# Kernel tuning notes

Measured on AMD Instinct MI355X. Metric: run time of the kernel, lower is better.

Reference implementation:

```python
import jax, jax.numpy as jnp
import numpy as np

B, S, HD = 2, 2048, 2048   # batch, seq_len, hidden_dim
NH = 16                    # num_heads
DH = HD // NH              # head_dim = 128
L = 512                    # kv_latent_dim
WINDOW = 128               # sliding window size
SINKS = 16                 # persistent (attention-sink) tokens
KTOP = 64                  # dynamic top-k tokens selected outside window/sinks
FORGET_P = 0.1             # stochastic forgetting probability


def setup_inputs() -> dict:
    key = jax.random.key(0)
    ks = jax.random.split(key, 7)
    s = 0.02
    x = jax.random.normal(ks[0], (B, S, HD), jnp.float32)
    Wq = jax.random.normal(ks[1], (HD, HD), jnp.float32) * s
    Wc = jax.random.normal(ks[2], (HD, L), jnp.float32) * s   # kv_latent_proj
    Wk = jax.random.normal(ks[3], (L, HD), jnp.float32) * s   # k_proj (latent -> hidden)
    Wv = jax.random.normal(ks[4], (L, HD), jnp.float32) * s   # v_proj (latent -> hidden)
    Wo = jax.random.normal(ks[5], (HD, HD), jnp.float32) * s  # out_proj
    forget_mask = jax.random.bernoulli(ks[6], FORGET_P, (B, NH, S, S))
    return dict(x=x, Wq=Wq, Wc=Wc, Wk=Wk, Wv=Wv, Wo=Wo, forget_mask=forget_mask)


def reference(x, Wq, Wc, Wk, Wv, Wo, forget_mask):
    scale = DH ** -0.5
    # projections: queries from x, keys/values through low-rank latent
    q = (x @ Wq).reshape(B, S, NH, DH).transpose(0, 2, 1, 3)   # [B,H,S,D]
    c = x @ Wc                                                  # [B,S,L] latent KV
    k = (c @ Wk).reshape(B, S, NH, DH).transpose(0, 2, 1, 3)
    v = (c @ Wv).reshape(B, S, NH, DH).transpose(0, 2, 1, 3)

    scores = jnp.einsum('bhqd,bhkd->bhqk', q, k) * scale        # [B,H,S,S]

    i = jnp.arange(S)[:, None]
    j = jnp.arange(S)[None, :]
    causal = j <= i
    # static pattern: sink tokens + sliding window (always attended)
    base = causal & ((j < SINKS) | ((i - j) < WINDOW))          # [S,S]

    NEG = jnp.finfo(scores.dtype).min
    # candidates for dynamic top-k: causal positions NOT already in window/sinks
    cand = jnp.where(causal & ~base, scores, NEG)
    vals, idx = jax.lax.top_k(cand, KTOP)                       # [B,H,S,K]

    # scatter top-k indices into a boolean mask (invalid = NEG-filled entries)
    N = B * NH * S
    rows = jnp.arange(N)[:, None]
    tk = jnp.zeros((N, S), dtype=bool).at[rows, idx.reshape(N, KTOP)].set(
        (vals > NEG / 2).reshape(N, KTOP))
    tk = tk.reshape(B, NH, S, S)

    # stochastic forgetting applies only to the dynamically selected tokens;
    # sinks and the sliding window are never forgotten
    allowed = base[None, None] | (tk & ~forget_mask)

    attn = jax.nn.softmax(jnp.where(allowed, scores, NEG), axis=-1)
    o = jnp.einsum('bhqk,bhkd->bhqd', attn, v)                  # [B,H,S,D]
    o = o.transpose(0, 2, 1, 3).reshape(B, S, HD)
    return o @ Wo
```

## Files before the change

kernel.cpp:

```cpp
#include <hip/hip_runtime.h>
#include <hip/hip_fp16.h>

#define B_ 2
#define S_ 2048
#define HD_ 2048
#define NH_ 16
#define DH_ 128
#define L_ 512
#define WINDOW_ 128
#define SINKS_ 16
#define KTOP_ 64
#define KST 2052

typedef __attribute__((ext_vector_type(4))) float f32x4;
typedef __attribute__((ext_vector_type(8))) __bf16 bf16x8;

__device__ inline unsigned short f2bf(float f) {
  unsigned int u = __float_as_uint(f);
  unsigned int r = (u + 0x7FFFu + ((u >> 16) & 1u)) >> 16;
  return (unsigned short)r;
}
__device__ inline float bf2f(unsigned short u) {
  unsigned int x = ((unsigned int)u) << 16;
  return __uint_as_float(x);
}
__device__ inline unsigned int mono(float f) {
  unsigned int u = __float_as_uint(f);
  return (u & 0x80000000u) ? ~u : (u | 0x80000000u);
}
__device__ inline float dq16(unsigned int k16) {
  unsigned int m = (k16 << 16) | 0x8000u;
  unsigned int u = (m & 0x80000000u) ? (m & 0x7fffffffu) : ~m;
  return __uint_as_float(u);
}
__device__ inline void gl16(const unsigned short* g, unsigned short* l) {
  __builtin_amdgcn_global_load_lds(
      (const __attribute__((address_space(1))) unsigned int*)g,
      (__attribute__((address_space(3))) unsigned int*)l, 16, 0, 0);
}

__global__ __launch_bounds__(256) void cast_f32(const float* __restrict__ in,
                                                unsigned short* __restrict__ hi,
                                                int n) {
  int i = (blockIdx.x * 256 + threadIdx.x) * 4;
  int stride = gridDim.x * 256 * 4;
  for (; i < n; i += stride) {
    float4 v = *(const float4*)(in + i);
    ushort4 h;
    h.x = f2bf(v.x); h.y = f2bf(v.y); h.z = f2bf(v.z); h.w = f2bf(v.w);
    *(ushort4*)(hi + i) = h;
  }
}

__global__ __launch_bounds__(256) void transpose_cast(const float* __restrict__ W,
                                                      unsigned short* __restrict__ WT,
                                                      int K, int N) {
  __shared__ unsigned short th[32][33];
  int n0 = blockIdx.x * 32, k0 = blockIdx.y * 32;
  int t = threadIdx.x;
  int cx = t & 31, ry = t >> 5;
#pragma unroll
  for (int it = 0; it < 4; ++it) {
    int kk = ry + it * 8;
    th[cx][kk] = f2bf(W[(size_t)(k0 + kk) * N + n0 + cx]);
  }
  __syncthreads();
#pragma unroll
  for (int it = 0; it < 4; ++it) {
    int nn = ry + it * 8;
    WT[(size_t)(n0 + nn) * K + k0 + cx] = th[nn][cx];
  }
}

__global__ __launch_bounds__(256) void transpose_split(const float* __restrict__ W,
                                                       unsigned short* __restrict__ WTh,
                                                       unsigned short* __restrict__ WTl,
                                                       int K, int N) {
  __shared__ unsigned short th[32][33];
  __shared__ unsigned short tl[32][33];
  int n0 = blockIdx.x * 32, k0 = blockIdx.y * 32;
  int t = threadIdx.x;
  int cx = t & 31, ry = t >> 5;
#pragma unroll
  for (int it = 0; it < 4; ++it) {
    int kk = ry + it * 8;
    float v = W[(size_t)(k0 + kk) * N + n0 + cx];
    unsigned short h = f2bf(v);
    th[cx][kk] = h;
    tl[cx][kk] = f2bf(v - bf2f(h));
  }
  __syncthreads();
#pragma unroll
  for (int it = 0; it < 4; ++it) {
    int nn = ry + it * 8;
    WTh[(size_t)(n0 + nn) * K + k0 + cx] = th[nn][cx];
    WTl[(size_t)(n0 + nn) * K + k0 + cx] = tl[nn][cx];
  }
}

__global__ __launch_bounds__(256) void gemm_c64(const unsigned short* __restrict__ Ah,
                                                const unsigned short* __restrict__ Bth,
                                                const unsigned short* __restrict__ Btl,
                                                unsigned short* __restrict__ Chi,
                                                int M, int N, int K) {
  __shared__ unsigned short lAh[64 * 32];
  __shared__ unsigned short lBh[128 * 32];
  __shared__ unsigned short lBl[128 * 32];
  int t = threadIdx.x;
  int row0 = blockIdx.x * 64, col0 = blockIdx.y * 128;
  int w = t >> 6, lane = t & 63;
  int wm = w >> 1, wn = w & 1;
  int lr = lane & 15, g = lane >> 4;

  f32x4 acc[2][4] = {};

  for (int kt = 0; kt < K; kt += 32) {
    {
      int Lb = w * 1024;
      int L = Lb + lane * 16;
      int rr = L >> 6, kc = (L & 63) >> 1;
      size_t offA = (size_t)(row0 + rr) * K + kt + kc;
      gl16(Ah + offA, lAh + Lb / 2);
      int Lb0 = (2 * w) * 1024;
      int L0 = Lb0 + lane * 16;
      int rr0 = L0 >> 6, kc0 = (L0 & 63) >> 1;
      size_t offB0 = (size_t)(col0 + rr0) * K + kt + kc0;
      gl16(Bth + offB0, lBh + Lb0 / 2);
      gl16(Btl + offB0, lBl + Lb0 / 2);
      int Lb1 = (2 * w + 1) * 1024;
      int L1 = Lb1 + lane * 16;
      int rr1 = L1 >> 6, kc1 = (L1 & 63) >> 1;
      size_t offB1 = (size_t)(col0 + rr1) * K + kt + kc1;
      gl16(Bth + offB1, lBh + Lb1 / 2);
      gl16(Btl + offB1, lBl + Lb1 / 2);
    }
    __syncthreads();
    bf16x8 af[2], bgh[4], bgl[4];
#pragma unroll
    for (int m = 0; m < 2; ++m)
      af[m] = *(const bf16x8*)&lAh[(wm * 32 + m * 16 + lr) * 32 + g * 8];
#pragma unroll
    for (int n = 0; n < 4; ++n) {
      bgh[n] = *(const bf16x8*)&lBh[(wn * 64 + n * 16 + lr) * 32 + g * 8];
      bgl[n] = *(const bf16x8*)&lBl[(wn * 64 + n * 16 + lr) * 32 + g * 8];
    }
#pragma unroll
    for (int m = 0; m < 2; ++m)
#pragma unroll
      for (int n = 0; n < 4; ++n) {
        acc[m][n] = __builtin_amdgcn_mfma_f32_16x16x32_bf16(af[m], bgh[n], acc[m][n], 0, 0, 0);
        acc[m][n] = __builtin_amdgcn_mfma_f32_16x16x32_bf16(af[m], bgl[n], acc[m][n], 0, 0, 0);
      }
    __syncthreads();
  }

#pragma unroll
  for (int m = 0; m < 2; ++m)
#pragma unroll
    for (int n = 0; n < 4; ++n)
#pragma unroll
      for (int r2 = 0; r2 < 4; ++r2) {
        int row = row0 + wm * 32 + m * 16 + g * 4 + r2;
        int col = col0 + wn * 64 + n * 16 + lr;
        Chi[(size_t)row * N + col] = f2bf(acc[m][n][r2]);
      }
}

__global__ __launch_bounds__(256) void gemm_1term(const unsigned short* __restrict__ Ah,
                                                  const unsigned short* __restrict__ Bth,
                                                  unsigned short* __restrict__ Chi,
                                                  int M, int N, int K, float oscale) {
  __shared__ unsigned short lA[128 * 32];
  __shared__ unsigned short lB[128 * 32];
  int t = threadIdx.x;
  int row0 = blockIdx.x * 128, col0 = blockIdx.y * 128;
  int w = t >> 6, lane = t & 63;
  int wm = w >> 1, wn = w & 1;
  int lr = lane & 15, g = lane >> 4;

  f32x4 acc[4][4] = {};

  for (int kt = 0; kt < K; kt += 32) {
#pragma unroll
    for (int cc = 0; cc < 2; ++cc) {
      int chunk = cc * 4 + w;
      int Lb = chunk * 1024;
      int L = Lb + lane * 16;
      int rr = L >> 6;
      int kc = (L & 63) >> 1;
      size_t offA = (size_t)(row0 + rr) * K + kt + kc;
      size_t offB = (size_t)(col0 + rr) * K + kt + kc;
      gl16(Ah + offA, lA + Lb / 2);
      gl16(Bth + offB, lB + Lb / 2);
    }
    __syncthreads();
    bf16x8 af[4], bg[4];
#pragma unroll
    for (int m = 0; m < 4; ++m) af[m] = *(const bf16x8*)&lA[(wm * 64 + m * 16 + lr) * 32 + g * 8];
#pragma unroll
    for (int n = 0; n < 4; ++n) bg[n] = *(const bf16x8*)&lB[(wn * 64 + n * 16 + lr) * 32 + g * 8];
#pragma unroll
    for (int m = 0; m < 4; ++m)
#pragma unroll
      for (int n = 0; n < 4; ++n)
        acc[m][n] = __builtin_amdgcn_mfma_f32_16x16x32_bf16(af[m], bg[n], acc[m][n], 0, 0, 0);
    __syncthreads();
  }

#pragma unroll
  for (int m = 0; m < 4; ++m)
#pragma unroll
    for (int n = 0; n < 4; ++n)
#pragma unroll
      for (int r2 = 0; r2 < 4; ++r2) {
        int row = row0 + wm * 64 + m * 16 + g * 4 + r2;
        int col = col0 + wn * 64 + n * 16 + lr;
        Chi[(size_t)row * N + col] = f2bf(acc[m][n][r2] * oscale);
      }
}

__global__ __launch_bounds__(256) void gemm_1h(const unsigned short* __restrict__ Ah,
                                               const unsigned short* __restrict__ Bth,
                                               unsigned short* __restrict__ Ch,
                                               int M, int N, int K) {
  __shared__ unsigned short lA[128 * 32];
  __shared__ unsigned short lB[128 * 32];
  int t = threadIdx.x;
  int row0 = blockIdx.x * 128, col0 = blockIdx.y * 128;
  int w = t >> 6, lane = t & 63;
  int wm = w >> 1, wn = w & 1;
  int lr = lane & 15, g = lane >> 4;

  f32x4 acc[4][4] = {};

  for (int kt = 0; kt < K; kt += 32) {
#pragma unroll
    for (int cc = 0; cc < 2; ++cc) {
      int chunk = cc * 4 + w;
      int Lb = chunk * 1024;
      int L = Lb + lane * 16;
      int rr = L >> 6;
      int kc = (L & 63) >> 1;
      size_t offA = (size_t)(row0 + rr) * K + kt + kc;
      size_t offB = (size_t)(col0 + rr) * K + kt + kc;
      gl16(Ah + offA, lA + Lb / 2);
      gl16(Bth + offB, lB + Lb / 2);
    }
    __syncthreads();
    bf16x8 af[4], bg[4];
#pragma unroll
    for (int m = 0; m < 4; ++m) af[m] = *(const bf16x8*)&lA[(wm * 64 + m * 16 + lr) * 32 + g * 8];
#pragma unroll
    for (int n = 0; n < 4; ++n) bg[n] = *(const bf16x8*)&lB[(wn * 64 + n * 16 + lr) * 32 + g * 8];
#pragma unroll
    for (int m = 0; m < 4; ++m)
#pragma unroll
      for (int n = 0; n < 4; ++n)
        acc[m][n] = __builtin_amdgcn_mfma_f32_16x16x32_bf16(af[m], bg[n], acc[m][n], 0, 0, 0);
    __syncthreads();
  }

#pragma unroll
  for (int m = 0; m < 4; ++m)
#pragma unroll
    for (int n = 0; n < 4; ++n)
#pragma unroll
      for (int r2 = 0; r2 < 4; ++r2) {
        int row = row0 + wm * 64 + m * 16 + g * 4 + r2;
        int col = col0 + wn * 64 + n * 16 + lr;
        __half hv = __float2half(acc[m][n][r2]);
        Ch[(size_t)row * N + col] = __half_as_ushort(hv);
      }
}

__global__ __launch_bounds__(256) void gemm_1f(const unsigned short* __restrict__ Ah,
                                               const unsigned short* __restrict__ Bth,
                                               float* __restrict__ Cf,
                                               int M, int N, int K) {
  __shared__ unsigned short lA[128 * 32];
  __shared__ unsigned short lB[128 * 32];
  int t = threadIdx.x;
  int row0 = blockIdx.x * 128, col0 = blockIdx.y * 128;
  int w = t >> 6, lane = t & 63;
  int wm = w >> 1, wn = w & 1;
  int lr = lane & 15, g = lane >> 4;

  f32x4 acc[4][4] = {};

  for (int kt = 0; kt < K; kt += 32) {
#pragma unroll
    for (int cc = 0; cc < 2; ++cc) {
      int chunk = cc * 4 + w;
      int Lb = chunk * 1024;
      int L = Lb + lane * 16;
      int rr = L >> 6;
      int kc = (L & 63) >> 1;
      size_t offA = (size_t)(row0 + rr) * K + kt + kc;
      size_t offB = (size_t)(col0 + rr) * K + kt + kc;
      gl16(Ah + offA, lA + Lb / 2);
      gl16(Bth + offB, lB + Lb / 2);
    }
    __syncthreads();
    bf16x8 af[4], bg[4];
#pragma unroll
    for (int m = 0; m < 4; ++m) af[m] = *(const bf16x8*)&lA[(wm * 64 + m * 16 + lr) * 32 + g * 8];
#pragma unroll
    for (int n = 0; n < 4; ++n) bg[n] = *(const bf16x8*)&lB[(wn * 64 + n * 16 + lr) * 32 + g * 8];
#pragma unroll
    for (int m = 0; m < 4; ++m)
#pragma unroll
      for (int n = 0; n < 4; ++n)
        acc[m][n] = __builtin_amdgcn_mfma_f32_16x16x32_bf16(af[m], bg[n], acc[m][n], 0, 0, 0);
    __syncthreads();
  }

#pragma unroll
  for (int m = 0; m < 4; ++m)
#pragma unroll
    for (int n = 0; n < 4; ++n)
#pragma unroll
      for (int r2 = 0; r2 < 4; ++r2) {
        int row = row0 + wm * 64 + m * 16 + g * 4 + r2;
        int col = col0 + wn * 64 + n * 16 + lr;
        Cf[(size_t)row * N + col] = acc[m][n][r2];
      }
}

__global__ __launch_bounds__(1024, 8) void attn_fused(const unsigned short* __restrict__ qh,
                                                      const unsigned short* __restrict__ kh,
                                                      const unsigned short* __restrict__ vhf,
                                                      const int* __restrict__ forget,
                                                      unsigned short* __restrict__ oh) {
  __shared__ unsigned short keys[16][KST];
  __shared__ unsigned int scratch[16][224];

  int bid = blockIdx.x;
  int bh = bid >> 7;
  int tile = 127 - (bid & 127);
  int b = bh >> 4, h = bh & 15;
  int i0 = tile * 16;
  int t = threadIdx.x;
  int w = t >> 6, lane = t & 63;
  int lr = lane & 15, g = lane >> 4;

  scratch[w][lane] = 0;
  scratch[w][lane + 64] = 0;
  __syncthreads();

  size_t qbase = ((size_t)(b * S_ + i0 + lr)) * HD_ + h * DH_;
  bf16x8 aq[4];
#pragma unroll
  for (int ks = 0; ks < 4; ++ks) aq[ks] = *(const bf16x8*)(qh + qbase + ks * 32 + g * 8);

  for (int kblk = w; kblk <= tile; kblk += 16) {
    int j0 = kblk * 16;
    size_t kbase = ((size_t)(b * S_ + j0 + lr)) * HD_ + h * DH_;
    f32x4 acc = {0.f, 0.f, 0.f, 0.f};
#pragma unroll
    for (int ks = 0; ks < 4; ++ks) {
      bf16x8 bk = *(const bf16x8*)(kh + kbase + ks * 32 + g * 8);
      acc = __builtin_amdgcn_mfma_f32_16x16x32_bf16(aq[ks], bk, acc, 0, 0, 0);
    }
    int j = j0 + lr;
#pragma unroll
    for (int r2 = 0; r2 < 4; ++r2) {
      int rr = g * 4 + r2;
      unsigned int k16 = mono(acc[r2]) >> 16;
      keys[rr][j] = (unsigned short)k16;
      int irow = i0 + rr;
      if (j >= SINKS_ && j <= irow - WINDOW_) {
        unsigned int bkt = k16 >> 8;
        atomicAdd(&scratch[rr][bkt >> 1], 1u << ((bkt & 1u) * 16));
      }
    }
  }
  __syncthreads();

  int r = w;
  int i = i0 + r;
  size_t rsg = (size_t)bh * S_ + i;

  int hi = i - WINDOW_;
  int C = hi - SINKS_ + 1;
  int mode = (C <= 0) ? 0 : (C <= KTOP_ ? 1 : 2);
  unsigned int T16 = 0; int neq = 0;

  if (mode == 2) {
    int cmax = hi >> 6;
    unsigned int need = KTOP_;
    unsigned int d0_, d1_;
    {
      unsigned int w0 = scratch[r][lane * 2], w1 = scratch[r][lane * 2 + 1];
      unsigned int s0 = (w0 & 0xffffu) + (w0 >> 16) + (w1 & 0xffffu) + (w1 >> 16);
      unsigned int suf = s0;
#pragma unroll
      for (int off = 1; off < 64; off <<= 1) {
        unsigned int vv = __shfl_down(suf, off);
        if (lane + off < 64) suf += vv;
      }
      unsigned int sufn = __shfl_down(suf, 1);
      if (lane == 63) sufn = 0;
      bool pl = (suf >= need) && (sufn < need);
      unsigned long long bal = __ballot(pl);
      int gg = __ffsll(bal) - 1;
      unsigned int basec = __shfl(sufn, gg);
      unsigned int cum = basec; int dstar = 4 * gg;
#pragma unroll
      for (int dd = 3; dd >= 0; --dd) {
        int d = 4 * gg + dd;
        unsigned int hd = (scratch[r][d >> 1] >> ((d & 1) * 16)) & 0xffffu;
        cum += hd;
        if (cum >= need) { dstar = d; break; }
      }
      unsigned int hstar = (scratch[r][dstar >> 1] >> ((dstar & 1) * 16)) & 0xffffu;
      need -= (cum - hstar);
      d0_ = (unsigned int)dstar;
    }
    scratch[r][lane] = 0; scratch[r][lane + 64] = 0;
    for (int c = 0; c <= cmax; ++c) {
      int j = c * 64 + lane;
      unsigned int key = keys[r][j];
      bool cand = (j >= SINKS_) && (j <= hi);
      if (cand && (key >> 8) == d0_) {
        unsigned int bkt = key & 255u;
        atomicAdd(&scratch[r][bkt >> 1], 1u << ((bkt & 1u) * 16));
      }
    }
    {
      unsigned int w0 = scratch[r][lane * 2], w1 = scratch[r][lane * 2 + 1];
      unsigned int s0 = (w0 & 0xffffu) + (w0 >> 16) + (w1 & 0xffffu) + (w1 >> 16);
      unsigned int suf = s0;
#pragma unroll
      for (int off = 1; off < 64; off <<= 1) {
        unsigned int vv = __shfl_down(suf, off);
        if (lane + off < 64) suf += vv;
      }
      unsigned int sufn = __shfl_down(suf, 1);
      if (lane == 63) sufn = 0;
      bool pl = (suf >= need) && (sufn < need);
      unsigned long long bal = __ballot(pl);
      int gg = __ffsll(bal) - 1;
      unsigned int basec = __shfl(sufn, gg);
      unsigned int cum = basec; int dstar = 4 * gg;
#pragma unroll
      for (int dd = 3; dd >= 0; --dd) {
        int d = 4 * gg + dd;
        unsigned int hd = (scratch[r][d >> 1] >> ((d & 1) * 16)) & 0xffffu;
        cum += hd;
        if (cum >= need) { dstar = d; break; }
      }
      unsigned int hstar = (scratch[r][dstar >> 1] >> ((dstar & 1) * 16)) & 0xffffu;
      need -= (cum - hstar);
      d1_ = (unsigned int)dstar;
    }
    T16 = (d0_ << 8) | d1_;
    neq = (int)need;
  }

  int neq_run = neq;
  int cnt = 0;
  float sum = 0.f;
  int nch = i >> 6;
  for (int c = 0; c <= nch; ++c) {
    int j = c * 64 + lane;
    bool valid = j <= i;
    unsigned int k16 = keys[r][j];
    bool isbase = valid && ((j < SINKS_) || ((i - j) < WINDOW_));
    bool iscand = valid && !isbase;
    bool sel = false, iseq = false;
    if (iscand) {
      if (mode == 1) sel = true;
      else if (mode == 2) {
        sel = k16 > T16;
        iseq = (k16 == T16);
      }
    }
    unsigned long long em = __ballot(iseq);
    if (iseq) {
      int rk = __popcll(em & ((1ull << lane) - 1ull));
      if (rk < neq_run) sel = true;
    }
    int taken = __popcll(em);
    neq_run -= (taken < neq_run) ? taken : neq_run;
    bool allowed = isbase || sel;
    float wgt = 0.f;
    if (allowed) { wgt = __expf(dq16(k16)); sum += wgt; }
    unsigned long long am = __ballot(allowed);
    if (allowed) {
      int pos = cnt + __popcll(am & ((1ull << lane) - 1ull));
      scratch[r][pos] = ((unsigned int)j << 16) |
                        (unsigned int)__half_as_ushort(__float2half(wgt));
    }
    cnt += __popcll(am);
  }

  float dropped = 0.f;
  {
    const int* frow = forget + rsg * (size_t)S_;
    int newcnt = 0;
    for (int c0 = 0; c0 < cnt; c0 += 64) {
      int p = c0 + lane;
      bool active = p < cnt;
      unsigned int pk = active ? scratch[r][p] : 0u;
      int j = (int)(pk >> 16);
      bool isb = (j < SINKS_) || ((i - j) < WINDOW_);
      bool fbit = false;
      if (active && !isb) fbit = (frow[j] != 0);
      if (fbit) dropped += __half2float(__ushort_as_half((unsigned short)(pk & 0xffffu)));
      bool keep = active && !fbit;
      unsigned long long km = __ballot(keep);
      if (keep) {
        int npos = newcnt + __popcll(km & ((1ull << lane) - 1ull));
        scratch[r][npos] = pk;
      }
      newcnt += __popcll(km);
    }
    cnt = newcnt;
  }

  float s2 = sum - dropped;
#pragma unroll
  for (int off = 32; off >= 1; off >>= 1) s2 += __shfl_xor(s2, off);
  float inv = 1.0f / s2;

  int quarter = lane >> 4;
  int q16 = lane & 15;
  int d0 = q16 * 8;
  int p0 = (cnt * quarter) >> 2;
  int p1 = (cnt * (quarter + 1)) >> 2;
  size_t vb0 = ((size_t)(b * S_)) * HD_ + h * DH_ + d0;

  __half2 A0 = __floats2half2_rn(0.f, 0.f);
  __half2 A1 = A0, A2 = A0, A3 = A0;
  int p = p0;
  for (; p + 2 <= p1; p += 2) {
    unsigned int pka = scratch[r][p], pkb = scratch[r][p + 1];
    int ja = (int)(pka >> 16), jb = (int)(pkb >> 16);
    __half2 wa = __half2half2(__ushort_as_half((unsigned short)(pka & 0xffffu)));
    __half2 wb = __half2half2(__ushort_as_half((unsigned short)(pkb & 0xffffu)));
    uint4 va = *(const uint4*)(vhf + vb0 + (size_t)ja * HD_);
    uint4 vb = *(const uint4*)(vhf + vb0 + (size_t)jb * HD_);
    A0 = __hfma2(wa, *(const __half2*)&va.x, A0);
    A1 = __hfma2(wa, *(const __half2*)&va.y, A1);
    A2 = __hfma2(wa, *(const __half2*)&va.z, A2);
    A3 = __hfma2(wa, *(const __half2*)&va.w, A3);
    A0 = __hfma2(wb, *(const __half2*)&vb.x, A0);
    A1 = __hfma2(wb, *(const __half2*)&vb.y, A1);
    A2 = __hfma2(wb, *(const __half2*)&vb.z, A2);
    A3 = __hfma2(wb, *(const __half2*)&vb.w, A3);
  }
  for (; p < p1; ++p) {
    unsigned int pk = scratch[r][p];
    int j = (int)(pk >> 16);
    __half2 w2 = __half2half2(__ushort_as_half((unsigned short)(pk & 0xffffu)));
    uint4 vj = *(const uint4*)(vhf + vb0 + (size_t)j * HD_);
    A0 = __hfma2(w2, *(const __half2*)&vj.x, A0);
    A1 = __hfma2(w2, *(const __half2*)&vj.y, A1);
    A2 = __hfma2(w2, *(const __half2*)&vj.z, A2);
    A3 = __hfma2(w2, *(const __half2*)&vj.w, A3);
  }
#pragma unroll
  for (int off = 16; off <= 32; off <<= 1) {
    int v0 = __shfl_xor(*(int*)&A0, off);
    int v1 = __shfl_xor(*(int*)&A1, off);
    int v2 = __shfl_xor(*(int*)&A2, off);
    int v3 = __shfl_xor(*(int*)&A3, off);
    A0 = __hadd2(A0, *(__half2*)&v0);
    A1 = __hadd2(A1, *(__half2*)&v1);
    A2 = __hadd2(A2, *(__half2*)&v2);
    A3 = __hadd2(A3, *(__half2*)&v3);
  }
  if (quarter == 0) {
    float2 f0 = __half22float2(A0), f1 = __half22float2(A1);
    float2 f2 = __half22float2(A2), f3 = __half22float2(A3);
    ushort4 h0, h1;
    h0.x = f2bf(f0.x * inv); h0.y = f2bf(f0.y * inv);
    h0.z = f2bf(f1.x * inv); h0.w = f2bf(f1.y * inv);
    h1.x = f2bf(f2.x * inv); h1.y = f2bf(f2.y * inv);
    h1.z = f2bf(f3.x * inv); h1.w = f2bf(f3.y * inv);
    size_t oidx = ((size_t)(b * S_ + i)) * HD_ + h * DH_ + d0;
    *(ushort4*)(oh + oidx) = h0;
    *(ushort4*)(oh + oidx + 4) = h1;
  }
}

extern "C" void kernel_launch(void* const* d_in, const int* in_sizes, int n_in,
                              void* d_out, int out_size, void* d_ws, size_t ws_size,
                              hipStream_t stream) {
  (void)in_sizes; (void)n_in; (void)out_size; (void)ws_size;
  const float* x  = (const float*)d_in[0];
  const float* Wq = (const float*)d_in[1];
  const float* Wc = (const float*)d_in[2];
  const float* Wk = (const float*)d_in[3];
  const float* Wv = (const float*)d_in[4];
  const float* Wo = (const float*)d_in[5];
  const int* forget = (const int*)d_in[6];

  char* ws = (char*)d_ws;
  size_t off = 0;
  auto alloc = [&](size_t bytes) { char* p = ws + off; off += (bytes + 255) & ~(size_t)255; return p; };

  unsigned short* x_bf = (unsigned short*)alloc((size_t)4096 * 2048 * 2);
  unsigned short* WqT  = (unsigned short*)alloc((size_t)2048 * 2048 * 2);
  unsigned short* WcTh = (unsigned short*)alloc((size_t)512 * 2048 * 2);
  unsigned short* WcTl = (unsigned short*)alloc((size_t)512 * 2048 * 2);
  unsigned short* WkT  = (unsigned short*)alloc((size_t)2048 * 512 * 2);
  unsigned short* WvT  = (unsigned short*)alloc((size_t)2048 * 512 * 2);
  unsigned short* WoT  = (unsigned short*)alloc((size_t)2048 * 2048 * 2);
  unsigned short* q_hi = (unsigned short*)alloc((size_t)4096 * 2048 * 2);
  unsigned short* c_hi = (unsigned short*)alloc((size_t)4096 * 512 * 2);
  unsigned short* k_hi = (unsigned short*)alloc((size_t)4096 * 2048 * 2);
  unsigned short* v_hf = (unsigned short*)alloc((size_t)4096 * 2048 * 2);

  unsigned short* o_hi = x_bf;

  const float scale = 0.08838834764831845f;

  cast_f32<<<2048, 256, 0, stream>>>(x, x_bf, 4096 * 2048);
  transpose_cast<<<dim3(64, 64), 256, 0, stream>>>(Wq, WqT, 2048, 2048);
  transpose_split<<<dim3(16, 64), 256, 0, stream>>>(Wc, WcTh, WcTl, 2048, 512);
  transpose_cast<<<dim3(64, 16), 256, 0, stream>>>(Wk, WkT, 512, 2048);
  transpose_cast<<<dim3(64, 16), 256, 0, stream>>>(Wv, WvT, 512, 2048);
  transpose_cast<<<dim3(64, 64), 256, 0, stream>>>(Wo, WoT, 2048, 2048);

  gemm_c64<<<dim3(64, 4), 256, 0, stream>>>(x_bf, WcTh, WcTl, c_hi, 4096, 512, 2048);
  gemm_1term<<<dim3(32, 16), 256, 0, stream>>>(x_bf, WqT, q_hi, 4096, 2048, 2048, scale);
  gemm_1term<<<dim3(32, 16), 256, 0, stream>>>(c_hi, WkT, k_hi, 4096, 2048, 512, 1.0f);
  gemm_1h<<<dim3(32, 16), 256, 0, stream>>>(c_hi, WvT, v_hf, 4096, 2048, 512);

  attn_fused<<<4096, 1024, 0, stream>>>(q_hi, k_hi, v_hf, forget, o_hi);

  gemm_1f<<<dim3(32, 16), 256, 0, stream>>>(o_hi, WoT, (float*)d_out, 4096, 2048, 2048);
}
```

Measured before the change: 596.1 us.

## Merge input prep kernels and specialize attention selection loop by chunk type

Replaces six cast/transpose launches with one prep_all kernel that dispatches on block index, removing per-launch overhead and idle gaps between small kernels. In the attention kernel, the candidate-selection loop gets fast paths for chunks that are fully base (window/sink) or fully candidate, which avoids per-lane base/candidate checks. Exponentials are moved out of that loop into a separate pass over only the kept entries after forgetting, so dropped tokens are never exponentiated. This adds an extra pass over the scratch list and more branching in the kernel.

```diff
diff --git a/kernel.cpp b/kernel.cpp
--- a/kernel.cpp
+++ b/kernel.cpp
@@ -39,25 +39,11 @@
       (__attribute__((address_space(3))) unsigned int*)l, 16, 0, 0);
 }
 
-__global__ __launch_bounds__(256) void cast_f32(const float* __restrict__ in,
-                                                unsigned short* __restrict__ hi,
-                                                int n) {
-  int i = (blockIdx.x * 256 + threadIdx.x) * 4;
-  int stride = gridDim.x * 256 * 4;
-  for (; i < n; i += stride) {
-    float4 v = *(const float4*)(in + i);
-    ushort4 h;
-    h.x = f2bf(v.x); h.y = f2bf(v.y); h.z = f2bf(v.z); h.w = f2bf(v.w);
-    *(ushort4*)(hi + i) = h;
-  }
-}
-
-__global__ __launch_bounds__(256) void transpose_cast(const float* __restrict__ W,
-                                                      unsigned short* __restrict__ WT,
-                                                      int K, int N) {
-  __shared__ unsigned short th[32][33];
-  int n0 = blockIdx.x * 32, k0 = blockIdx.y * 32;
-  int t = threadIdx.x;
+__device__ inline void trans_cast_dev(const float* __restrict__ W,
+                                      unsigned short* __restrict__ WT,
+                                      int K, int N, int bx, int by, int t,
+                                      unsigned short th[32][33]) {
+  int n0 = bx * 32, k0 = by * 32;
   int cx = t & 31, ry = t >> 5;
 #pragma unroll
   for (int it = 0; it < 4; ++it) {
@@ -72,14 +58,13 @@
   }
 }
 
-__global__ __launch_bounds__(256) void transpose_split(const float* __restrict__ W,
-                                                       unsigned short* __restrict__ WTh,
-                                                       unsigned short* __restrict__ WTl,
-                                                       int K, int N) {
-  __shared__ unsigned short th[32][33];
-  __shared__ unsigned short tl[32][33];
-  int n0 = blockIdx.x * 32, k0 = blockIdx.y * 32;
-  int t = threadIdx.x;
+__device__ inline void trans_split_dev(const float* __restrict__ W,
+                                       unsigned short* __restrict__ WTh,
+                                       unsigned short* __restrict__ WTl,
+                                       int K, int N, int bx, int by, int t,
+                                       unsigned short th[32][33],
+                                       unsigned short tl[32][33]) {
+  int n0 = bx * 32, k0 = by * 32;
   int cx = t & 31, ry = t >> 5;
 #pragma unroll
   for (int it = 0; it < 4; ++it) {
@@ -95,6 +80,50 @@
     int nn = ry + it * 8;
     WTh[(size_t)(n0 + nn) * K + k0 + cx] = th[nn][cx];
     WTl[(size_t)(n0 + nn) * K + k0 + cx] = tl[nn][cx];
+  }
+}
+
+__global__ __launch_bounds__(256) void prep_all(const float* __restrict__ x,
+                                                const float* __restrict__ Wq,
+                                                const float* __restrict__ Wc,
+                                                const float* __restrict__ Wk,
+                                                const float* __restrict__ Wv,
+                                                const float* __restrict__ Wo,
+                                                unsigned short* __restrict__ x_bf,
+                                                unsigned short* __restrict__ WqT,
+                                                unsigned short* __restrict__ WcTh,
+                                                unsigned short* __restrict__ WcTl,
+                                                unsigned short* __restrict__ WkT,
+                                                unsigned short* __restrict__ WvT,
+                                                unsigned short* __restrict__ WoT) {
+  __shared__ unsigned short th[32][33];
+  __shared__ unsigned short tl[32][33];
+  int bid = blockIdx.x;
+  int t = threadIdx.x;
+  if (bid < 2048) {
+    const int n = 4096 * 2048;
+    const int stride = 2048 * 256 * 4;
+    for (int i = (bid * 256 + t) * 4; i < n; i += stride) {
+      float4 v = *(const float4*)(x + i);
+      ushort4 h;
+      h.x = f2bf(v.x); h.y = f2bf(v.y); h.z = f2bf(v.z); h.w = f2bf(v.w);
+      *(ushort4*)(x_bf + i) = h;
+    }
+  } else if (bid < 2048 + 4096) {
+    int bb = bid - 2048;
+    trans_cast_dev(Wq, WqT, 2048, 2048, bb & 63, bb >> 6, t, th);
+  } else if (bid < 2048 + 4096 + 1024) {
+    int bb = bid - (2048 + 4096);
+    trans_split_dev(Wc, WcTh, WcTl, 2048, 512, bb & 15, bb >> 4, t, th, tl);
+  } else if (bid < 2048 + 4096 + 2048) {
+    int bb = bid - (2048 + 4096 + 1024);
+    trans_cast_dev(Wk, WkT, 512, 2048, bb & 63, bb >> 6, t, th);
+  } else if (bid < 2048 + 4096 + 3072) {
+    int bb = bid - (2048 + 4096 + 2048);
+    trans_cast_dev(Wv, WvT, 512, 2048, bb & 63, bb >> 6, t, th);
+  } else {
+    int bb = bid - (2048 + 4096 + 3072);
+    trans_cast_dev(Wo, WoT, 2048, 2048, bb & 63, bb >> 6, t, th);
   }
 }
 
@@ -459,42 +488,61 @@
 
   int neq_run = neq;
   int cnt = 0;
-  float sum = 0.f;
   int nch = i >> 6;
+  int cfull_end = (mode == 2) ? ((hi + 1) >> 6) : 0;
   for (int c = 0; c <= nch; ++c) {
     int j = c * 64 + lane;
-    bool valid = j <= i;
-    unsigned int k16 = keys[r][j];
-    bool isbase = valid && ((j < SINKS_) || ((i - j) < WINDOW_));
-    bool iscand = valid && !isbase;
-    bool sel = false, iseq = false;
-    if (iscand) {
-      if (mode == 1) sel = true;
-      else if (mode == 2) {
-        sel = k16 > T16;
-        iseq = (k16 == T16);
-      }
-    }
-    unsigned long long em = __ballot(iseq);
-    if (iseq) {
-      int rk = __popcll(em & ((1ull << lane) - 1ull));
-      if (rk < neq_run) sel = true;
-    }
-    int taken = __popcll(em);
-    neq_run -= (taken < neq_run) ? taken : neq_run;
-    bool allowed = isbase || sel;
-    float wgt = 0.f;
-    if (allowed) { wgt = __expf(dq16(k16)); sum += wgt; }
-    unsigned long long am = __ballot(allowed);
-    if (allowed) {
-      int pos = cnt + __popcll(am & ((1ull << lane) - 1ull));
-      scratch[r][pos] = ((unsigned int)j << 16) |
-                        (unsigned int)__half_as_ushort(__float2half(wgt));
-    }
-    cnt += __popcll(am);
-  }
-
-  float dropped = 0.f;
+    unsigned int k16v = keys[r][j];
+    if (mode != 2 || c * 64 > hi) {
+      bool allowed = j <= i;
+      unsigned long long am = __ballot(allowed);
+      if (allowed) {
+        int pos = cnt + __popcll(am & ((1ull << lane) - 1ull));
+        scratch[r][pos] = ((unsigned int)j << 16) | k16v;
+      }
+      cnt += __popcll(am);
+    } else if (c >= 1 && c < cfull_end) {
+      bool sel = k16v > T16;
+      bool iseq = (k16v == T16);
+      unsigned long long em = __ballot(iseq);
+      if (iseq) {
+        int rk = __popcll(em & ((1ull << lane) - 1ull));
+        if (rk < neq_run) sel = true;
+      }
+      int taken = __popcll(em);
+      neq_run -= (taken < neq_run) ? taken : neq_run;
+      unsigned long long am = __ballot(sel);
+      if (sel) {
+        int pos = cnt + __popcll(am & ((1ull << lane) - 1ull));
+        scratch[r][pos] = ((unsigned int)j << 16) | k16v;
+      }
+      cnt += __popcll(am);
+    } else {
+      bool valid = j <= i;
+      bool isbase = valid && ((j < SINKS_) || ((i - j) < WINDOW_));
+      bool iscand = valid && !isbase;
+      bool sel = false, iseq = false;
+      if (iscand) {
+        sel = k16v > T16;
+        iseq = (k16v == T16);
+      }
+      unsigned long long em = __ballot(iseq);
+      if (iseq) {
+        int rk = __popcll(em & ((1ull << lane) - 1ull));
+        if (rk < neq_run) sel = true;
+      }
+      int taken = __popcll(em);
+      neq_run -= (taken < neq_run) ? taken : neq_run;
+      bool allowed = isbase || sel;
+      unsigned long long am = __ballot(allowed);
+      if (allowed) {
+        int pos = cnt + __popcll(am & ((1ull << lane) - 1ull));
+        scratch[r][pos] = ((unsigned int)j << 16) | k16v;
+      }
+      cnt += __popcll(am);
+    }
+  }
+
   {
     const int* frow = forget + rsg * (size_t)S_;
     int newcnt = 0;
@@ -506,7 +554,6 @@
       bool isb = (j < SINKS_) || ((i - j) < WINDOW_);
       bool fbit = false;
       if (active && !isb) fbit = (frow[j] != 0);
-      if (fbit) dropped += __half2float(__ushort_as_half((unsigned short)(pk & 0xffffu)));
       bool keep = active && !fbit;
       unsigned long long km = __ballot(keep);
       if (keep) {
@@ -518,10 +565,17 @@
     cnt = newcnt;
   }
 
-  float s2 = sum - dropped;
-#pragma unroll
-  for (int off = 32; off >= 1; off >>= 1) s2 += __shfl_xor(s2, off);
-  float inv = 1.0f / s2;
+  float sum = 0.f;
+  for (int p = lane; p < cnt; p += 64) {
+    unsigned int pk = scratch[r][p];
+    float wgt = __expf(dq16(pk & 0xffffu));
+    sum += wgt;
+    scratch[r][p] = (pk & 0xffff0000u) |
+                    (unsigned int)__half_as_ushort(__float2half(wgt));
+  }
+#pragma unroll
+  for (int off = 32; off >= 1; off >>= 1) sum += __shfl_xor(sum, off);
+  float inv = 1.0f / sum;
 
   int quarter = lane >> 4;
   int q16 = lane & 15;
@@ -616,12 +670,8 @@
 
   const float scale = 0.08838834764831845f;
 
-  cast_f32<<<2048, 256, 0, stream>>>(x, x_bf, 4096 * 2048);
-  transpose_cast<<<dim3(64, 64), 256, 0, stream>>>(Wq, WqT, 2048, 2048);
-  transpose_split<<<dim3(16, 64), 256, 0, stream>>>(Wc, WcTh, WcTl, 2048, 512);
-  transpose_cast<<<dim3(64, 16), 256, 0, stream>>>(Wk, WkT, 512, 2048);
-  transpose_cast<<<dim3(64, 16), 256, 0, stream>>>(Wv, WvT, 512, 2048);
-  transpose_cast<<<dim3(64, 64), 256, 0, stream>>>(Wo, WoT, 2048, 2048);
+  prep_all<<<13312, 256, 0, stream>>>(x, Wq, Wc, Wk, Wv, Wo,
+                                      x_bf, WqT, WcTh, WcTl, WkT, WvT, WoT);
 
   gemm_c64<<<dim3(64, 4), 256, 0, stream>>>(x_bf, WcTh, WcTl, c_hi, 4096, 512, 2048);
   gemm_1term<<<dim3(32, 16), 256, 0, stream>>>(x_bf, WqT, q_hi, 4096, 2048, 2048, scale);
```

New measurement: 583.4 us. 1.02x faster.
